# Performance work log

Measured on AMD Instinct MI355X. Metric: run time of the kernel, lower is better.

Reference implementation:

```python
import jax, jax.numpy as jnp
import numpy as np

N, E, F_IN, HID, OUT, N_ROOTS = 100000, 1600000, 128, 128, 64, 1024


def _lin_params(key, fan_in, fan_out):
    k1, k2 = jax.random.split(key)
    s = 1.0 / np.sqrt(fan_in)
    w = jax.random.uniform(k1, (fan_in, fan_out), jnp.float32, -s, s)
    b = jax.random.uniform(k2, (fan_out,), jnp.float32, -s, s)
    return w, b


def setup_inputs() -> dict:
    key = jax.random.key(0)
    ks = jax.random.split(key, 16)
    x = jax.random.normal(ks[0], (N, F_IN), jnp.float32)
    edge_index = jax.random.randint(ks[1], (2, E), 0, N, jnp.int64)
    root_idx = jax.random.randint(ks[2], (N_ROOTS,), 0, N, jnp.int64)
    # GINConv MLPs: Linear(in,out) -> ReLU -> Linear(out,out); train_eps=True (init 0)
    w0a, b0a = _lin_params(ks[3], F_IN, HID)
    w0b, b0b = _lin_params(ks[4], HID, HID)
    w1a, b1a = _lin_params(ks[5], HID, HID)
    w1b, b1b = _lin_params(ks[6], HID, HID)
    w2a, b2a = _lin_params(ks[7], HID, OUT)
    w2b, b2b = _lin_params(ks[8], OUT, OUT)
    z = jnp.zeros((), jnp.float32)
    return dict(x=x, edge_index=edge_index, root_idx=root_idx,
                eps0=z, w0a=w0a, b0a=b0a, w0b=w0b, b0b=b0b,
                eps1=z, w1a=w1a, b1a=b1a, w1b=w1b, b1b=b1b,
                eps2=z, w2a=w2a, b2a=b2a, w2b=w2b, b2b=b2b)


def _gin_conv(x, edge_index, eps, w1, b1, w2, b2):
    src, dst = edge_index[0], edge_index[1]
    # sum_{j in N(i)} x_j : gather source features, scatter-add to destinations
    agg = jax.ops.segment_sum(x[src], dst, num_segments=x.shape[0])
    h = (1.0 + eps) * x + agg
    h = jnp.maximum(h @ w1 + b1, 0.0)
    return h @ w2 + b2


def reference(x, edge_index, root_idx,
              eps0, w0a, b0a, w0b, b0b,
              eps1, w1a, b1a, w1b, b1b,
              eps2, w2a, b2a, w2b, b2b):
    h = jnp.maximum(_gin_conv(x, edge_index, eps0, w0a, b0a, w0b, b0b), 0.0)
    h = jnp.maximum(_gin_conv(h, edge_index, eps1, w1a, b1a, w1b, b1b), 0.0)
    # dropout is identity at inference (self.training == False)
    h = _gin_conv(h, edge_index, eps2, w2a, b2a, w2b, b2b)
    return h[root_idx]  # [N_ROOTS, OUT] == x[root_mask]
```

## Files before the change

kernel.cpp:

```cpp
#include <hip/hip_runtime.h>


typedef __bf16  bf16x8 __attribute__((ext_vector_type(8)));
typedef float   f32x4  __attribute__((ext_vector_type(4)));

#define NBINS 784
#define BCAP  38
#define CAP   8192
#define LDR   136

__global__ __launch_bounds__(1024) void k_scatter(const int* __restrict__ src,
                                                  const int* __restrict__ dst,
                                                  int* __restrict__ gcnt,
                                                  int* __restrict__ realcnt,
                                                  unsigned* __restrict__ ebuf,
                                                  int e, int nb,
                                                  const float4* __restrict__ xf,
                                                  unsigned short* __restrict__ xb,
                                                  long n8,
                                                  const float* __restrict__ w0a,
                                                  const float* __restrict__ w0b,
                                                  const float* __restrict__ w1a,
                                                  const float* __restrict__ w1b,
                                                  unsigned short* __restrict__ wT,
                                                  const int* __restrict__ roots,
                                                  int nr,
                                                  int* __restrict__ af_root) {
    __shared__ unsigned lbuf[NBINS * BCAP];
    __shared__ int lcnt[NBINS];
    __shared__ int sbase[NBINS];
    const int t = threadIdx.x;
    for (int b = t; b < nb; b += 1024) lcnt[b] = 0;

    {
        int gi = blockIdx.x * 1024 + t;
        if (gi < nr) af_root[roots[gi]] = 1;
    }
    {
        int gi = blockIdx.x * 1024 + t;
        if (gi < 65536) {
            int m = gi >> 14, j = gi & 16383;
            const float* w = (m == 0) ? w0a : (m == 1) ? w0b : (m == 2) ? w1a : w1b;
            int k = j >> 7, n = j & 127;
            *(__bf16*)&wT[m * 16384 + n * 128 + k] = (__bf16)w[j];
        }
    }
    for (long i = (long)blockIdx.x * 1024 + t; i < n8; i += 262144) {
        float4 a = xf[2 * i], b = xf[2 * i + 1];
        bf16x8 v;
        v[0] = (__bf16)a.x; v[1] = (__bf16)a.y; v[2] = (__bf16)a.z; v[3] = (__bf16)a.w;
        v[4] = (__bf16)b.x; v[5] = (__bf16)b.y; v[6] = (__bf16)b.z; v[7] = (__bf16)b.w;
        *(bf16x8*)&xb[i * 8] = v;
    }
    __syncthreads();

    const int per = (((e + 255) / 256) + 7) & ~7;
    const int beg = blockIdx.x * per;
    const int end = (beg + per < e) ? beg + per : e;

    for (int base = beg; base < end; base += 8192) {
        int i0 = base + t * 8;
        if (i0 >= end) continue;
        if (i0 + 8 <= end) {
            int4 s0 = *(const int4*)&src[i0];
            int4 s1 = *(const int4*)&src[i0 + 4];
            int4 d0 = *(const int4*)&dst[i0];
            int4 d1 = *(const int4*)&dst[i0 + 4];
            int ss[8] = {s0.x, s0.y, s0.z, s0.w, s1.x, s1.y, s1.z, s1.w};
            int dd[8] = {d0.x, d0.y, d0.z, d0.w, d1.x, d1.y, d1.z, d1.w};
#pragma unroll
            for (int q = 0; q < 8; ++q) {
                int b = dd[q] >> 7;
                int p = atomicAdd(&lcnt[b], 1);
                if (p < BCAP)
                    lbuf[b * BCAP + p] =
                        (unsigned)ss[q] | ((unsigned)(dd[q] & 127) << 17);
            }
        } else {
            int lim = (i0 + 8 < end) ? i0 + 8 : end;
            for (int i = i0; i < lim; ++i) {
                int d = dst[i];
                int b = d >> 7;
                int p = atomicAdd(&lcnt[b], 1);
                if (p < BCAP)
                    lbuf[b * BCAP + p] =
                        (unsigned)src[i] | ((unsigned)(d & 127) << 17);
            }
        }
    }
    __syncthreads();

    for (int b = t; b < nb; b += 1024) {
        int r = lcnt[b]; if (r > BCAP) r = BCAP;
        int bb = 0;
        if (r > 0) {
            int nf = (r + 15) & ~15;
            bb = atomicAdd(&gcnt[b * 16], nf);
            atomicAdd(&realcnt[b], r);
        }
        sbase[b] = bb;
    }
    __syncthreads();

    const int wave = t >> 6, lane = t & 63;
    const int gidx = wave * 4 + (lane >> 4), sub = lane & 15;
    for (int b = gidx; b < nb; b += 64) {
        int r = lcnt[b]; if (r > BCAP) r = BCAP;
        if (r == 0) continue;
        int nf = (r + 15) & ~15;
        int base2 = sbase[b];
        unsigned* cell = ebuf + (size_t)b * CAP;
        for (int j = sub; j < nf; j += 16) {
            unsigned v = (j < r) ? lbuf[b * BCAP + j] : 0xFFFFFFFFu;
            if (base2 + j < CAP) cell[base2 + j] = v;
        }
    }
}

__global__ __launch_bounds__(1024) void k_bscan(const int* __restrict__ realcnt,
                                                int* __restrict__ boff,
                                                int* __restrict__ rp,
                                                int nb, int n, int e) {
    __shared__ int sh[1024];
    int t = threadIdx.x;
    sh[t] = (t < nb) ? realcnt[t] : 0;
    __syncthreads();
    for (int off = 1; off < 1024; off <<= 1) {
        int u = (t >= off) ? sh[t - off] : 0;
        __syncthreads();
        sh[t] += u;
        __syncthreads();
    }
    if (t < nb) boff[t] = (t == 0) ? 0 : sh[t - 1];
    if (t == 0) rp[n] = e;
}

__global__ __launch_bounds__(512) void k_build(const unsigned* __restrict__ ebuf,
                                               const int* __restrict__ gcnt,
                                               const int* __restrict__ boff,
                                               int* __restrict__ rp,
                                               int* __restrict__ csr,
                                               const int* __restrict__ af_root,
                                               int* __restrict__ af, int n) {
    __shared__ int bins[128];
    __shared__ int incl[128];
    __shared__ int cur[128];
    __shared__ unsigned char isroot[128];
    int b = blockIdx.x, t = threadIdx.x;
    if (t < 128) {
        bins[t] = 0;
        int node = b * 128 + t;
        unsigned char ir = (node < n && af_root[node]) ? 1 : 0;
        isroot[t] = ir;
        if (ir) af[node] = 1;
    }
    __syncthreads();
    int c = gcnt[b * 16]; if (c > CAP) c = CAP;
    const unsigned* seg = ebuf + ((size_t)b * CAP);
    for (int j = t; j < c; j += 512) {
        unsigned w = seg[j];
        if (w != 0xFFFFFFFFu) atomicAdd(&bins[(w >> 17) & 127], 1);
    }
    __syncthreads();
    if (t < 128) incl[t] = bins[t];
    __syncthreads();
    for (int off = 1; off < 128; off <<= 1) {
        int u = (t < 128 && t >= off) ? incl[t - off] : 0;
        __syncthreads();
        if (t < 128) incl[t] += u;
        __syncthreads();
    }
    int base = boff[b];
    if (t < 128) {
        int ex = (t == 0) ? 0 : incl[t - 1];
        cur[t] = ex;
        int node = b * 128 + t;
        if (node < n) rp[node] = base + ex;
    }
    __syncthreads();
    for (int j = t; j < c; j += 512) {
        unsigned w = seg[j];
        if (w != 0xFFFFFFFFu) {
            int ldst = (w >> 17) & 127;
            int s = (int)(w & 0x1FFFF);
            int slot = atomicAdd(&cur[ldst], 1);
            csr[base + slot] = s;
            if (isroot[ldst]) af[s] = 1;
        }
    }
}

__global__ void k_compact(const int* __restrict__ af, int* __restrict__ list,
                          int* __restrict__ cnt, int n) {
    int i = blockIdx.x * blockDim.x + threadIdx.x;
    if (i < n && af[i]) {
        int p = atomicAdd(cnt, 1);
        list[p] = i;
    }
}

__global__ __launch_bounds__(256) void k_segz(const unsigned short* __restrict__ xb,
                                              const int* __restrict__ rp,
                                              const int* __restrict__ csr,
                                              const float* __restrict__ epsp,
                                              unsigned short* __restrict__ zout,
                                              const int* __restrict__ list,
                                              const int* __restrict__ cntp, int n) {
    int gid = blockIdx.x * 256 + threadIdx.x;
    int j = gid >> 4, lane = gid & 15;
    int rows = n;
    if (cntp) { int c = *cntp; rows = c < n ? c : n; }
    if (j >= rows) return;
    int node = list ? list[j] : j;
    int b = rp[node], e = rp[node + 1];
    float s0[8], s1[8];
#pragma unroll
    for (int q = 0; q < 8; ++q) { s0[q] = 0.f; s1[q] = 0.f; }
    int k = b;
    for (; k + 1 < e; k += 2) {
        bf16x8 v0 = *(const bf16x8*)&xb[(size_t)csr[k]     * 128 + lane * 8];
        bf16x8 v1 = *(const bf16x8*)&xb[(size_t)csr[k + 1] * 128 + lane * 8];
#pragma unroll
        for (int q = 0; q < 8; ++q) { s0[q] += (float)v0[q]; s1[q] += (float)v1[q]; }
    }
    if (k < e) {
        bf16x8 v0 = *(const bf16x8*)&xb[(size_t)csr[k] * 128 + lane * 8];
#pragma unroll
        for (int q = 0; q < 8; ++q) s0[q] += (float)v0[q];
    }
    const float epsv = 1.0f + epsp[0];
    bf16x8 xv = *(const bf16x8*)&xb[(size_t)node * 128 + lane * 8];
    bf16x8 o;
#pragma unroll
    for (int q = 0; q < 8; ++q)
        o[q] = (__bf16)(epsv * (float)xv[q] + s0[q] + s1[q]);
    *(bf16x8*)&zout[(size_t)j * 128 + lane * 8] = o;
}

__global__ __launch_bounds__(256) void k_mlp(const unsigned short* __restrict__ zbuf,
                                             const unsigned short* __restrict__ w1T,
                                             const float* __restrict__ b1,
                                             const unsigned short* __restrict__ w2T,
                                             const float* __restrict__ b2,
                                             unsigned short* __restrict__ out,
                                             const int* __restrict__ list,
                                             const int* __restrict__ cntp, int nrows) {
    __shared__ unsigned short zt[128 * LDR];
    const int t = threadIdx.x;
    int rows = nrows;
    if (cntp) { int c = *cntp; rows = c < nrows ? c : nrows; }
    const int row0 = blockIdx.x * 128;
    if (row0 >= rows) return;

    for (int i = t; i < 2048; i += 256) {
        int r = i >> 4, c = i & 15;
        int g = row0 + r;
        bf16x8 zv;
        if (g < rows) {
            zv = *(const bf16x8*)&zbuf[(size_t)g * 128 + c * 8];
        } else {
#pragma unroll
            for (int q = 0; q < 8; ++q) zv[q] = (__bf16)0.0f;
        }
        *(bf16x8*)&zt[r * LDR + c * 8] = zv;
    }
    __syncthreads();

    const int lane = t & 63;
    const int wm = (t >> 7) & 1, wn = (t >> 6) & 1;
    const int lr = lane & 15, lk = lane >> 4;

    f32x4 zero4 = {0.f, 0.f, 0.f, 0.f};
    f32x4 acc[4][4];
#pragma unroll
    for (int mt = 0; mt < 4; ++mt)
#pragma unroll
        for (int nt = 0; nt < 4; ++nt) acc[mt][nt] = zero4;

#pragma unroll
    for (int kb = 0; kb < 4; ++kb) {
        const int c = kb * 4 + lk;
        bf16x8 a[4];
#pragma unroll
        for (int mt = 0; mt < 4; ++mt)
            a[mt] = *(const bf16x8*)&zt[(wm * 64 + mt * 16 + lr) * LDR + c * 8];
#pragma unroll
        for (int nt = 0; nt < 4; ++nt) {
            bf16x8 b = *(const bf16x8*)&w1T[(wn * 64 + nt * 16 + lr) * 128 + c * 8];
#pragma unroll
            for (int mt = 0; mt < 4; ++mt)
                acc[mt][nt] = __builtin_amdgcn_mfma_f32_16x16x32_bf16(a[mt], b, acc[mt][nt], 0, 0, 0);
        }
    }
    __syncthreads();

#pragma unroll
    for (int nt = 0; nt < 4; ++nt) {
        int col = wn * 64 + nt * 16 + lr;
        float bv = b1[col];
#pragma unroll
        for (int mt = 0; mt < 4; ++mt)
#pragma unroll
            for (int q = 0; q < 4; ++q) {
                int hr = wm * 64 + mt * 16 + lk * 4 + q;
                float hv = fmaxf(acc[mt][nt][q] + bv, 0.f);
                *(__bf16*)&zt[hr * LDR + col] = (__bf16)hv;
            }
    }
    __syncthreads();

    f32x4 acc2[4][4];
#pragma unroll
    for (int mt = 0; mt < 4; ++mt)
#pragma unroll
        for (int nt = 0; nt < 4; ++nt) acc2[mt][nt] = zero4;
#pragma unroll
    for (int kb = 0; kb < 4; ++kb) {
        const int c = kb * 4 + lk;
        bf16x8 a[4];
#pragma unroll
        for (int mt = 0; mt < 4; ++mt)
            a[mt] = *(const bf16x8*)&zt[(wm * 64 + mt * 16 + lr) * LDR + c * 8];
#pragma unroll
        for (int nt = 0; nt < 4; ++nt) {
            bf16x8 b = *(const bf16x8*)&w2T[(wn * 64 + nt * 16 + lr) * 128 + c * 8];
#pragma unroll
            for (int mt = 0; mt < 4; ++mt)
                acc2[mt][nt] = __builtin_amdgcn_mfma_f32_16x16x32_bf16(a[mt], b, acc2[mt][nt], 0, 0, 0);
        }
    }
    __syncthreads();

#pragma unroll
    for (int nt = 0; nt < 4; ++nt) {
        int col = wn * 64 + nt * 16 + lr;
        float bv = b2[col];
#pragma unroll
        for (int mt = 0; mt < 4; ++mt)
#pragma unroll
            for (int q = 0; q < 4; ++q) {
                int orow = wm * 64 + mt * 16 + lk * 4 + q;
                float ov = fmaxf(acc2[mt][nt][q] + bv, 0.f);
                *(__bf16*)&zt[orow * LDR + col] = (__bf16)ov;
            }
    }
    __syncthreads();

    for (int i = t; i < 2048; i += 256) {
        int r = i >> 4, c = i & 15;
        int g = row0 + r;
        if (g < rows) {
            int node = list ? list[g] : g;
            *(bf16x8*)&out[(size_t)node * 128 + c * 8] =
                *(const bf16x8*)&zt[r * LDR + c * 8];
        }
    }
}

__global__ __launch_bounds__(128) void k_root(const unsigned short* __restrict__ x2,
                                              const int* __restrict__ rp,
                                              const int* __restrict__ csr,
                                              const int* __restrict__ roots,
                                              const float* __restrict__ epsp,
                                              const float* __restrict__ wa,
                                              const float* __restrict__ ba,
                                              const float* __restrict__ wb,
                                              const float* __restrict__ bb,
                                              float* __restrict__ out) {
    __shared__ float hin[128];
    __shared__ float h[64];
    int r = blockIdx.x, t = threadIdx.x;
    int node = roots[r];
    float s = (1.0f + epsp[0]) * (float)(*(const __bf16*)&x2[(size_t)node * 128 + t]);
    int b = rp[node], e = rp[node + 1];
    for (int k = b; k < e; ++k)
        s += (float)(*(const __bf16*)&x2[(size_t)csr[k] * 128 + t]);
    hin[t] = s;
    __syncthreads();
    if (t < 64) {
        float a = ba[t];
        for (int k = 0; k < 128; ++k) a += hin[k] * wa[k * 64 + t];
        h[t] = fmaxf(a, 0.f);
    }
    __syncthreads();
    if (t < 64) {
        float a = bb[t];
        for (int k = 0; k < 64; ++k) a += h[k] * wb[k * 64 + t];
        out[(size_t)r * 64 + t] = a;
    }
}

extern "C" void kernel_launch(void* const* d_in, const int* in_sizes, int n_in,
                              void* d_out, int out_size, void* d_ws, size_t ws_size,
                              hipStream_t stream) {
    const float* x    = (const float*)d_in[0];
    const int*   ei   = (const int*)d_in[1];
    const int*   root = (const int*)d_in[2];
    const float* eps0 = (const float*)d_in[3];
    const float* w0a  = (const float*)d_in[4];
    const float* b0a  = (const float*)d_in[5];
    const float* w0b  = (const float*)d_in[6];
    const float* b0b  = (const float*)d_in[7];
    const float* eps1 = (const float*)d_in[8];
    const float* w1a  = (const float*)d_in[9];
    const float* b1a  = (const float*)d_in[10];
    const float* w1b  = (const float*)d_in[11];
    const float* b1b  = (const float*)d_in[12];
    const float* eps2 = (const float*)d_in[13];
    const float* w2a  = (const float*)d_in[14];
    const float* b2a  = (const float*)d_in[15];
    const float* w2b  = (const float*)d_in[16];
    const float* b2b  = (const float*)d_in[17];

    const int N  = in_sizes[0] / 128;
    const int E  = in_sizes[1] / 2;
    const int NR = in_sizes[2];
    const int MAXACT = 65536;
    const int NB = (N + 127) / 128;
    const int* src = ei;
    const int* dst = ei + E;

    char* p = (char*)d_ws;
    unsigned short* xb = (unsigned short*)p; p += (size_t)N * 128 * 2;
    unsigned short* x1 = (unsigned short*)p; p += (size_t)N * 128 * 2;
    unsigned short* z0 = (unsigned short*)p; p += (size_t)N * 128 * 2;
    char* shared0 = p;
    size_t ebuf_bytes = (size_t)NB * CAP * 4;
    size_t x2_bytes   = (size_t)N * 128 * 2;
    p += (ebuf_bytes > x2_bytes ? ebuf_bytes : x2_bytes);
    unsigned*       ebuf = (unsigned*)shared0;
    unsigned short* x2   = (unsigned short*)shared0;
    unsigned short* z1   = (unsigned short*)p; p += (size_t)MAXACT * 128 * 2;
    unsigned short* wT   = (unsigned short*)p; p += 4 * 128 * 128 * 2;
    int* rp      = (int*)p; p += (size_t)(N + 64) * 4;
    int* list    = (int*)p; p += (size_t)(N + 64) * 4;
    int* boff    = (int*)p; p += 4096;
    char* zbeg = p;
    int* af      = (int*)p; p += (size_t)(N + 64) * 4;
    int* af_root = (int*)p; p += (size_t)(N + 64) * 4;
    int* cnt     = (int*)p; p += 256;
    int* gcnt    = (int*)p; p += (size_t)NB * 16 * 4;
    int* realcnt = (int*)p; p += (size_t)(NB + 64) * 4;
    size_t zbytes = (size_t)(p - zbeg);
    int* csr     = (int*)p; p += (size_t)E * 4;
    unsigned short* w0aT = wT;
    unsigned short* w0bT = wT + 16384;
    unsigned short* w1aT = wT + 32768;
    unsigned short* w1bT = wT + 49152;

    hipMemsetAsync(zbeg, 0, zbytes, stream);
    k_scatter<<<256, 1024, 0, stream>>>(src, dst, gcnt, realcnt, ebuf, E, NB,
                                        (const float4*)x, xb, (long)N * 16,
                                        w0a, w0b, w1a, w1b, wT,
                                        root, NR, af_root);
    k_bscan<<<1, 1024, 0, stream>>>(realcnt, boff, rp, NB, N, E);
    k_build<<<NB, 512, 0, stream>>>(ebuf, gcnt, boff, rp, csr, af_root, af, N);
    k_compact<<<(N + 255) / 256, 256, 0, stream>>>(af, list, cnt, N);

    k_segz<<<(N * 16 + 255) / 256, 256, 0, stream>>>(xb, rp, csr, eps0, z0,
                                                     nullptr, nullptr, N);
    k_mlp<<<(N + 127) / 128, 256, 0, stream>>>(z0, w0aT, b0a, w0bT, b0b,
                                               x1, nullptr, nullptr, N);
    k_segz<<<(MAXACT * 16 + 255) / 256, 256, 0, stream>>>(x1, rp, csr, eps1, z1,
                                                          list, cnt, MAXACT);
    k_mlp<<<(MAXACT + 127) / 128, 256, 0, stream>>>(z1, w1aT, b1a, w1bT, b1b,
                                                    x2, list, cnt, MAXACT);
    k_root<<<NR, 128, 0, stream>>>(x2, rp, csr, root, eps2, w2a, b2a, w2b, b2b,
                                   (float*)d_out);
}
```

Measured before the change: 212.9 us.

## Fuse neighbor aggregation into GIN MLP kernel with 16-row tiles

Merges the gather/segment-sum kernel into the two-layer MLP kernel, so each block aggregates 16 node rows straight into shared memory and runs both MFMA GEMMs on them. This removes the round trip of the intermediate z buffers through global memory and one kernel launch per layer. The tile shrinks from 128 to 16 rows, with each wave owning 32 output columns, so weights are reread from global/L2 by many more blocks and there is less MFMA reuse per weight load. Gather latency and matrix work now share the same blocks, with a launch-bounds occupancy hint added to keep enough blocks resident.

```diff
diff --git a/kernel.cpp b/kernel.cpp
--- a/kernel.cpp
+++ b/kernel.cpp
@@ -199,155 +199,112 @@
     }
 }
 
-__global__ __launch_bounds__(256) void k_segz(const unsigned short* __restrict__ xb,
-                                              const int* __restrict__ rp,
-                                              const int* __restrict__ csr,
-                                              const float* __restrict__ epsp,
-                                              unsigned short* __restrict__ zout,
-                                              const int* __restrict__ list,
-                                              const int* __restrict__ cntp, int n) {
-    int gid = blockIdx.x * 256 + threadIdx.x;
-    int j = gid >> 4, lane = gid & 15;
-    int rows = n;
-    if (cntp) { int c = *cntp; rows = c < n ? c : n; }
-    if (j >= rows) return;
-    int node = list ? list[j] : j;
-    int b = rp[node], e = rp[node + 1];
-    float s0[8], s1[8];
-#pragma unroll
-    for (int q = 0; q < 8; ++q) { s0[q] = 0.f; s1[q] = 0.f; }
-    int k = b;
-    for (; k + 1 < e; k += 2) {
-        bf16x8 v0 = *(const bf16x8*)&xb[(size_t)csr[k]     * 128 + lane * 8];
-        bf16x8 v1 = *(const bf16x8*)&xb[(size_t)csr[k + 1] * 128 + lane * 8];
-#pragma unroll
-        for (int q = 0; q < 8; ++q) { s0[q] += (float)v0[q]; s1[q] += (float)v1[q]; }
-    }
-    if (k < e) {
-        bf16x8 v0 = *(const bf16x8*)&xb[(size_t)csr[k] * 128 + lane * 8];
-#pragma unroll
-        for (int q = 0; q < 8; ++q) s0[q] += (float)v0[q];
-    }
-    const float epsv = 1.0f + epsp[0];
-    bf16x8 xv = *(const bf16x8*)&xb[(size_t)node * 128 + lane * 8];
-    bf16x8 o;
-#pragma unroll
-    for (int q = 0; q < 8; ++q)
-        o[q] = (__bf16)(epsv * (float)xv[q] + s0[q] + s1[q]);
-    *(bf16x8*)&zout[(size_t)j * 128 + lane * 8] = o;
-}
-
-__global__ __launch_bounds__(256) void k_mlp(const unsigned short* __restrict__ zbuf,
-                                             const unsigned short* __restrict__ w1T,
-                                             const float* __restrict__ b1,
-                                             const unsigned short* __restrict__ w2T,
-                                             const float* __restrict__ b2,
-                                             unsigned short* __restrict__ out,
-                                             const int* __restrict__ list,
-                                             const int* __restrict__ cntp, int nrows) {
-    __shared__ unsigned short zt[128 * LDR];
+__global__ __launch_bounds__(256, 6) void k_gmlp(const unsigned short* __restrict__ xb,
+                                                 const int* __restrict__ rp,
+                                                 const int* __restrict__ csr,
+                                                 const float* __restrict__ epsp,
+                                                 const unsigned short* __restrict__ w1T,
+                                                 const float* __restrict__ b1,
+                                                 const unsigned short* __restrict__ w2T,
+                                                 const float* __restrict__ b2,
+                                                 unsigned short* __restrict__ out,
+                                                 const int* __restrict__ list,
+                                                 const int* __restrict__ cntp, int nrows) {
+    __shared__ unsigned short zt[16 * LDR];
+    __shared__ unsigned short ht[16 * LDR];
     const int t = threadIdx.x;
     int rows = nrows;
     if (cntp) { int c = *cntp; rows = c < nrows ? c : nrows; }
-    const int row0 = blockIdx.x * 128;
+    const int row0 = blockIdx.x * 16;
     if (row0 >= rows) return;
 
-    for (int i = t; i < 2048; i += 256) {
-        int r = i >> 4, c = i & 15;
-        int g = row0 + r;
+    {
+        const int r16 = t >> 4, lane16 = t & 15;
+        int j = row0 + r16;
         bf16x8 zv;
-        if (g < rows) {
-            zv = *(const bf16x8*)&zbuf[(size_t)g * 128 + c * 8];
+        if (j < rows) {
+            int node = list ? list[j] : j;
+            int b = rp[node], e = rp[node + 1];
+            float s[8];
+#pragma unroll
+            for (int q = 0; q < 8; ++q) s[q] = 0.f;
+            int k = b;
+            for (; k + 1 < e; k += 2) {
+                bf16x8 v0 = *(const bf16x8*)&xb[(size_t)csr[k]     * 128 + lane16 * 8];
+                bf16x8 v1 = *(const bf16x8*)&xb[(size_t)csr[k + 1] * 128 + lane16 * 8];
+#pragma unroll
+                for (int q = 0; q < 8; ++q) s[q] += (float)v0[q] + (float)v1[q];
+            }
+            if (k < e) {
+                bf16x8 v0 = *(const bf16x8*)&xb[(size_t)csr[k] * 128 + lane16 * 8];
+#pragma unroll
+                for (int q = 0; q < 8; ++q) s[q] += (float)v0[q];
+            }
+            const float epsv = 1.0f + epsp[0];
+            bf16x8 xv = *(const bf16x8*)&xb[(size_t)node * 128 + lane16 * 8];
+#pragma unroll
+            for (int q = 0; q < 8; ++q)
+                zv[q] = (__bf16)(epsv * (float)xv[q] + s[q]);
         } else {
 #pragma unroll
             for (int q = 0; q < 8; ++q) zv[q] = (__bf16)0.0f;
         }
-        *(bf16x8*)&zt[r * LDR + c * 8] = zv;
+        *(bf16x8*)&zt[(t >> 4) * LDR + (t & 15) * 8] = zv;
     }
     __syncthreads();
 
     const int lane = t & 63;
-    const int wm = (t >> 7) & 1, wn = (t >> 6) & 1;
+    const int wave = t >> 6;
     const int lr = lane & 15, lk = lane >> 4;
+    const int n0 = wave * 32;
 
     f32x4 zero4 = {0.f, 0.f, 0.f, 0.f};
-    f32x4 acc[4][4];
-#pragma unroll
-    for (int mt = 0; mt < 4; ++mt)
-#pragma unroll
-        for (int nt = 0; nt < 4; ++nt) acc[mt][nt] = zero4;
-
+    f32x4 acc[2] = {zero4, zero4};
 #pragma unroll
     for (int kb = 0; kb < 4; ++kb) {
-        const int c = kb * 4 + lk;
-        bf16x8 a[4];
-#pragma unroll
-        for (int mt = 0; mt < 4; ++mt)
-            a[mt] = *(const bf16x8*)&zt[(wm * 64 + mt * 16 + lr) * LDR + c * 8];
-#pragma unroll
-        for (int nt = 0; nt < 4; ++nt) {
-            bf16x8 b = *(const bf16x8*)&w1T[(wn * 64 + nt * 16 + lr) * 128 + c * 8];
-#pragma unroll
-            for (int mt = 0; mt < 4; ++mt)
-                acc[mt][nt] = __builtin_amdgcn_mfma_f32_16x16x32_bf16(a[mt], b, acc[mt][nt], 0, 0, 0);
-        }
-    }
-    __syncthreads();
-
-#pragma unroll
-    for (int nt = 0; nt < 4; ++nt) {
-        int col = wn * 64 + nt * 16 + lr;
+        bf16x8 a = *(const bf16x8*)&zt[lr * LDR + (kb * 4 + lk) * 8];
+#pragma unroll
+        for (int nt = 0; nt < 2; ++nt) {
+            bf16x8 b = *(const bf16x8*)&w1T[(size_t)(n0 + nt * 16 + lr) * 128 + (kb * 4 + lk) * 8];
+            acc[nt] = __builtin_amdgcn_mfma_f32_16x16x32_bf16(a, b, acc[nt], 0, 0, 0);
+        }
+    }
+#pragma unroll
+    for (int nt = 0; nt < 2; ++nt) {
+        int col = n0 + nt * 16 + lr;
         float bv = b1[col];
 #pragma unroll
-        for (int mt = 0; mt < 4; ++mt)
-#pragma unroll
-            for (int q = 0; q < 4; ++q) {
-                int hr = wm * 64 + mt * 16 + lk * 4 + q;
-                float hv = fmaxf(acc[mt][nt][q] + bv, 0.f);
-                *(__bf16*)&zt[hr * LDR + col] = (__bf16)hv;
-            }
-    }
-    __syncthreads();
-
-    f32x4 acc2[4][4];
-#pragma unroll
-    for (int mt = 0; mt < 4; ++mt)
-#pragma unroll
-        for (int nt = 0; nt < 4; ++nt) acc2[mt][nt] = zero4;
+        for (int q = 0; q < 4; ++q) {
+            float hv = fmaxf(acc[nt][q] + bv, 0.f);
+            *(__bf16*)&ht[(lk * 4 + q) * LDR + col] = (__bf16)hv;
+        }
+    }
+    __syncthreads();
+
+    f32x4 acc2[2] = {zero4, zero4};
 #pragma unroll
     for (int kb = 0; kb < 4; ++kb) {
-        const int c = kb * 4 + lk;
-        bf16x8 a[4];
-#pragma unroll
-        for (int mt = 0; mt < 4; ++mt)
-            a[mt] = *(const bf16x8*)&zt[(wm * 64 + mt * 16 + lr) * LDR + c * 8];
-#pragma unroll
-        for (int nt = 0; nt < 4; ++nt) {
-            bf16x8 b = *(const bf16x8*)&w2T[(wn * 64 + nt * 16 + lr) * 128 + c * 8];
-#pragma unroll
-            for (int mt = 0; mt < 4; ++mt)
-                acc2[mt][nt] = __builtin_amdgcn_mfma_f32_16x16x32_bf16(a[mt], b, acc2[mt][nt], 0, 0, 0);
-        }
-    }
-    __syncthreads();
-
-#pragma unroll
-    for (int nt = 0; nt < 4; ++nt) {
-        int col = wn * 64 + nt * 16 + lr;
+        bf16x8 a = *(const bf16x8*)&ht[lr * LDR + (kb * 4 + lk) * 8];
+#pragma unroll
+        for (int nt = 0; nt < 2; ++nt) {
+            bf16x8 b = *(const bf16x8*)&w2T[(size_t)(n0 + nt * 16 + lr) * 128 + (kb * 4 + lk) * 8];
+            acc2[nt] = __builtin_amdgcn_mfma_f32_16x16x32_bf16(a, b, acc2[nt], 0, 0, 0);
+        }
+    }
+#pragma unroll
+    for (int nt = 0; nt < 2; ++nt) {
+        int col = n0 + nt * 16 + lr;
         float bv = b2[col];
 #pragma unroll
-        for (int mt = 0; mt < 4; ++mt)
-#pragma unroll
-            for (int q = 0; q < 4; ++q) {
-                int orow = wm * 64 + mt * 16 + lk * 4 + q;
-                float ov = fmaxf(acc2[mt][nt][q] + bv, 0.f);
-                *(__bf16*)&zt[orow * LDR + col] = (__bf16)ov;
-            }
-    }
-    __syncthreads();
-
-    for (int i = t; i < 2048; i += 256) {
-        int r = i >> 4, c = i & 15;
+        for (int q = 0; q < 4; ++q) {
+            float ov = fmaxf(acc2[nt][q] + bv, 0.f);
+            *(__bf16*)&zt[(lk * 4 + q) * LDR + col] = (__bf16)ov;
+        }
+    }
+    __syncthreads();
+
+    {
+        int r = t >> 4, c = t & 15;
         int g = row0 + r;
         if (g < rows) {
             int node = list ? list[g] : g;
@@ -423,14 +380,12 @@
     char* p = (char*)d_ws;
     unsigned short* xb = (unsigned short*)p; p += (size_t)N * 128 * 2;
     unsigned short* x1 = (unsigned short*)p; p += (size_t)N * 128 * 2;
-    unsigned short* z0 = (unsigned short*)p; p += (size_t)N * 128 * 2;
     char* shared0 = p;
     size_t ebuf_bytes = (size_t)NB * CAP * 4;
     size_t x2_bytes   = (size_t)N * 128 * 2;
     p += (ebuf_bytes > x2_bytes ? ebuf_bytes : x2_bytes);
     unsigned*       ebuf = (unsigned*)shared0;
     unsigned short* x2   = (unsigned short*)shared0;
-    unsigned short* z1   = (unsigned short*)p; p += (size_t)MAXACT * 128 * 2;
     unsigned short* wT   = (unsigned short*)p; p += 4 * 128 * 128 * 2;
     int* rp      = (int*)p; p += (size_t)(N + 64) * 4;
     int* list    = (int*)p; p += (size_t)(N + 64) * 4;
@@ -457,14 +412,12 @@
     k_build<<<NB, 512, 0, stream>>>(ebuf, gcnt, boff, rp, csr, af_root, af, N);
     k_compact<<<(N + 255) / 256, 256, 0, stream>>>(af, list, cnt, N);
 
-    k_segz<<<(N * 16 + 255) / 256, 256, 0, stream>>>(xb, rp, csr, eps0, z0,
-                                                     nullptr, nullptr, N);
-    k_mlp<<<(N + 127) / 128, 256, 0, stream>>>(z0, w0aT, b0a, w0bT, b0b,
-                                               x1, nullptr, nullptr, N);
-    k_segz<<<(MAXACT * 16 + 255) / 256, 256, 0, stream>>>(x1, rp, csr, eps1, z1,
-                                                          list, cnt, MAXACT);
-    k_mlp<<<(MAXACT + 127) / 128, 256, 0, stream>>>(z1, w1aT, b1a, w1bT, b1b,
-                                                    x2, list, cnt, MAXACT);
+    k_gmlp<<<(N + 15) / 16, 256, 0, stream>>>(xb, rp, csr, eps0,
+                                              w0aT, b0a, w0bT, b0b,
+                                              x1, nullptr, nullptr, N);
+    k_gmlp<<<(MAXACT + 15) / 16, 256, 0, stream>>>(x1, rp, csr, eps1,
+                                                   w1aT, b1a, w1bT, b1b,
+                                                   x2, list, cnt, MAXACT);
     k_root<<<NR, 128, 0, stream>>>(x2, rp, csr, root, eps2, w2a, b2a, w2b, b2b,
                                    (float*)d_out);
 }
```

Result: no change. 209.9 us (-1.4%).

## Fuse layer-1 neighbor aggregation with MLP into single kernel over active nodes

Applied to the files above, without the earlier changes.

Adds k_gmlp, which computes the GIN aggregation for 16 active nodes per block straight into shared memory and then runs both MFMA linear layers. This removes the z1 intermediate buffer and one kernel launch for layer 1. k_segz and k_mlp lose their list/count indirection because they now serve only the dense layer 0. The cost is small 16-row tiles, so weights are read from global memory by every block and MFMA reuse drops; launch bounds request 6 blocks per CU to keep occupancy up.

```diff
diff --git a/kernel.cpp b/kernel.cpp
--- a/kernel.cpp
+++ b/kernel.cpp
@@ -204,15 +204,11 @@
                                               const int* __restrict__ csr,
                                               const float* __restrict__ epsp,
                                               unsigned short* __restrict__ zout,
-                                              const int* __restrict__ list,
-                                              const int* __restrict__ cntp, int n) {
+                                              int n) {
     int gid = blockIdx.x * 256 + threadIdx.x;
     int j = gid >> 4, lane = gid & 15;
-    int rows = n;
-    if (cntp) { int c = *cntp; rows = c < n ? c : n; }
-    if (j >= rows) return;
-    int node = list ? list[j] : j;
-    int b = rp[node], e = rp[node + 1];
+    if (j >= n) return;
+    int b = rp[j], e = rp[j + 1];
     float s0[8], s1[8];
 #pragma unroll
     for (int q = 0; q < 8; ++q) { s0[q] = 0.f; s1[q] = 0.f; }
@@ -229,7 +225,7 @@
         for (int q = 0; q < 8; ++q) s0[q] += (float)v0[q];
     }
     const float epsv = 1.0f + epsp[0];
-    bf16x8 xv = *(const bf16x8*)&xb[(size_t)node * 128 + lane * 8];
+    bf16x8 xv = *(const bf16x8*)&xb[(size_t)j * 128 + lane * 8];
     bf16x8 o;
 #pragma unroll
     for (int q = 0; q < 8; ++q)
@@ -243,20 +239,17 @@
                                              const unsigned short* __restrict__ w2T,
                                              const float* __restrict__ b2,
                                              unsigned short* __restrict__ out,
-                                             const int* __restrict__ list,
-                                             const int* __restrict__ cntp, int nrows) {
+                                             int nrows) {
     __shared__ unsigned short zt[128 * LDR];
     const int t = threadIdx.x;
-    int rows = nrows;
-    if (cntp) { int c = *cntp; rows = c < nrows ? c : nrows; }
     const int row0 = blockIdx.x * 128;
-    if (row0 >= rows) return;
+    if (row0 >= nrows) return;
 
     for (int i = t; i < 2048; i += 256) {
         int r = i >> 4, c = i & 15;
         int g = row0 + r;
         bf16x8 zv;
-        if (g < rows) {
+        if (g < nrows) {
             zv = *(const bf16x8*)&zbuf[(size_t)g * 128 + c * 8];
         } else {
 #pragma unroll
@@ -348,6 +341,119 @@
 
     for (int i = t; i < 2048; i += 256) {
         int r = i >> 4, c = i & 15;
+        int g = row0 + r;
+        if (g < nrows)
+            *(bf16x8*)&out[(size_t)g * 128 + c * 8] =
+                *(const bf16x8*)&zt[r * LDR + c * 8];
+    }
+}
+
+__global__ __launch_bounds__(256, 6) void k_gmlp(const unsigned short* __restrict__ xb,
+                                                 const int* __restrict__ rp,
+                                                 const int* __restrict__ csr,
+                                                 const float* __restrict__ epsp,
+                                                 const unsigned short* __restrict__ w1T,
+                                                 const float* __restrict__ b1,
+                                                 const unsigned short* __restrict__ w2T,
+                                                 const float* __restrict__ b2,
+                                                 unsigned short* __restrict__ out,
+                                                 const int* __restrict__ list,
+                                                 const int* __restrict__ cntp, int nrows) {
+    __shared__ unsigned short zt[16 * LDR];
+    __shared__ unsigned short ht[16 * LDR];
+    const int t = threadIdx.x;
+    int rows = nrows;
+    if (cntp) { int c = *cntp; rows = c < nrows ? c : nrows; }
+    const int row0 = blockIdx.x * 16;
+    if (row0 >= rows) return;
+
+    {
+        const int r16 = t >> 4, lane16 = t & 15;
+        int j = row0 + r16;
+        bf16x8 zv;
+        if (j < rows) {
+            int node = list ? list[j] : j;
+            int b = rp[node], e = rp[node + 1];
+            float s[8];
+#pragma unroll
+            for (int q = 0; q < 8; ++q) s[q] = 0.f;
+            int k = b;
+            for (; k + 1 < e; k += 2) {
+                bf16x8 v0 = *(const bf16x8*)&xb[(size_t)csr[k]     * 128 + lane16 * 8];
+                bf16x8 v1 = *(const bf16x8*)&xb[(size_t)csr[k + 1] * 128 + lane16 * 8];
+#pragma unroll
+                for (int q = 0; q < 8; ++q) s[q] += (float)v0[q] + (float)v1[q];
+            }
+            if (k < e) {
+                bf16x8 v0 = *(const bf16x8*)&xb[(size_t)csr[k] * 128 + lane16 * 8];
+#pragma unroll
+                for (int q = 0; q < 8; ++q) s[q] += (float)v0[q];
+            }
+            const float epsv = 1.0f + epsp[0];
+            bf16x8 xv = *(const bf16x8*)&xb[(size_t)node * 128 + lane16 * 8];
+#pragma unroll
+            for (int q = 0; q < 8; ++q)
+                zv[q] = (__bf16)(epsv * (float)xv[q] + s[q]);
+        } else {
+#pragma unroll
+            for (int q = 0; q < 8; ++q) zv[q] = (__bf16)0.0f;
+        }
+        *(bf16x8*)&zt[(t >> 4) * LDR + (t & 15) * 8] = zv;
+    }
+    __syncthreads();
+
+    const int lane = t & 63;
+    const int wave = t >> 6;
+    const int lr = lane & 15, lk = lane >> 4;
+    const int n0 = wave * 32;
+
+    f32x4 zero4 = {0.f, 0.f, 0.f, 0.f};
+    f32x4 acc[2] = {zero4, zero4};
+#pragma unroll
+    for (int kb = 0; kb < 4; ++kb) {
+        bf16x8 a = *(const bf16x8*)&zt[lr * LDR + (kb * 4 + lk) * 8];
+#pragma unroll
+        for (int nt = 0; nt < 2; ++nt) {
+            bf16x8 b = *(const bf16x8*)&w1T[(size_t)(n0 + nt * 16 + lr) * 128 + (kb * 4 + lk) * 8];
+            acc[nt] = __builtin_amdgcn_mfma_f32_16x16x32_bf16(a, b, acc[nt], 0, 0, 0);
+        }
+    }
+#pragma unroll
+    for (int nt = 0; nt < 2; ++nt) {
+        int col = n0 + nt * 16 + lr;
+        float bv = b1[col];
+#pragma unroll
+        for (int q = 0; q < 4; ++q) {
+            float hv = fmaxf(acc[nt][q] + bv, 0.f);
+            *(__bf16*)&ht[(lk * 4 + q) * LDR + col] = (__bf16)hv;
+        }
+    }
+    __syncthreads();
+
+    f32x4 acc2[2] = {zero4, zero4};
+#pragma unroll
+    for (int kb = 0; kb < 4; ++kb) {
+        bf16x8 a = *(const bf16x8*)&ht[lr * LDR + (kb * 4 + lk) * 8];
+#pragma unroll
+        for (int nt = 0; nt < 2; ++nt) {
+            bf16x8 b = *(const bf16x8*)&w2T[(size_t)(n0 + nt * 16 + lr) * 128 + (kb * 4 + lk) * 8];
+            acc2[nt] = __builtin_amdgcn_mfma_f32_16x16x32_bf16(a, b, acc2[nt], 0, 0, 0);
+        }
+    }
+#pragma unroll
+    for (int nt = 0; nt < 2; ++nt) {
+        int col = n0 + nt * 16 + lr;
+        float bv = b2[col];
+#pragma unroll
+        for (int q = 0; q < 4; ++q) {
+            float ov = fmaxf(acc2[nt][q] + bv, 0.f);
+            *(__bf16*)&zt[(lk * 4 + q) * LDR + col] = (__bf16)ov;
+        }
+    }
+    __syncthreads();
+
+    {
+        int r = t >> 4, c = t & 15;
         int g = row0 + r;
         if (g < rows) {
             int node = list ? list[g] : g;
@@ -430,7 +536,6 @@
     p += (ebuf_bytes > x2_bytes ? ebuf_bytes : x2_bytes);
     unsigned*       ebuf = (unsigned*)shared0;
     unsigned short* x2   = (unsigned short*)shared0;
-    unsigned short* z1   = (unsigned short*)p; p += (size_t)MAXACT * 128 * 2;
     unsigned short* wT   = (unsigned short*)p; p += 4 * 128 * 128 * 2;
     int* rp      = (int*)p; p += (size_t)(N + 64) * 4;
     int* list    = (int*)p; p += (size_t)(N + 64) * 4;
@@ -457,14 +562,11 @@
     k_build<<<NB, 512, 0, stream>>>(ebuf, gcnt, boff, rp, csr, af_root, af, N);
     k_compact<<<(N + 255) / 256, 256, 0, stream>>>(af, list, cnt, N);
 
-    k_segz<<<(N * 16 + 255) / 256, 256, 0, stream>>>(xb, rp, csr, eps0, z0,
-                                                     nullptr, nullptr, N);
-    k_mlp<<<(N + 127) / 128, 256, 0, stream>>>(z0, w0aT, b0a, w0bT, b0b,
-                                               x1, nullptr, nullptr, N);
-    k_segz<<<(MAXACT * 16 + 255) / 256, 256, 0, stream>>>(x1, rp, csr, eps1, z1,
-                                                          list, cnt, MAXACT);
-    k_mlp<<<(MAXACT + 127) / 128, 256, 0, stream>>>(z1, w1aT, b1a, w1bT, b1b,
-                                                    x2, list, cnt, MAXACT);
+    k_segz<<<(N * 16 + 255) / 256, 256, 0, stream>>>(xb, rp, csr, eps0, z0, N);
+    k_mlp<<<(N + 127) / 128, 256, 0, stream>>>(z0, w0aT, b0a, w0bT, b0b, x1, N);
+    k_gmlp<<<(MAXACT + 15) / 16, 256, 0, stream>>>(x1, rp, csr, eps1,
+                                                   w1aT, b1a, w1bT, b1b,
+                                                   x2, list, cnt, MAXACT);
     k_root<<<NR, 128, 0, stream>>>(x2, rp, csr, root, eps2, w2a, b2a, w2b, b2b,
                                    (float*)d_out);
 }
```

Result: faster. 203.2 us (-4.6%).
